# Optimization experiments

Hardware: AMD Instinct MI355X
Metric: run time of the kernel (lower is better)

Reference implementation:

```python
import jax, jax.numpy as jnp
import numpy as np

B, K, H, W = 8, 1024, 24, 24
C = H * W            # in_channels = 576
NH = 6               # hardcoded num_heads
HD = C // NH         # 96


def setup_inputs() -> dict:
    key = jax.random.key(0)
    ks = jax.random.split(key, 8)
    s = 1.0 / np.sqrt(C)
    return {
        "input1": jax.random.normal(ks[0], (B, K, H, W), jnp.float32),
        "input2": jax.random.normal(ks[1], (B, K, H, W), jnp.float32),
        "Wq": jax.random.uniform(ks[2], (C, C), jnp.float32, -s, s),
        "bq": jax.random.uniform(ks[3], (C,), jnp.float32, -s, s),
        "Wk": jax.random.uniform(ks[4], (C, C), jnp.float32, -s, s),
        "bk": jax.random.uniform(ks[5], (C,), jnp.float32, -s, s),
        "Wv": jax.random.uniform(ks[6], (C, C), jnp.float32, -s, s),
        "bv": jax.random.uniform(ks[7], (C,), jnp.float32, -s, s),
    }


def reference(input1, input2, Wq, bq, Wk, bk, Wv, bv):
    b, k, h, w = input1.shape
    c = h * w
    x1 = input1.reshape(b, k, c)
    x2 = input2.reshape(b, k, c)
    # torch nn.Linear: y = x @ W^T + b
    q = x1 @ Wq.T + bq                      # [b, k, c]
    kk = x2 @ Wk.T + bk
    v = x2 @ Wv.T + bv
    # torch .view scrambles: [b, k, c] -> [b, NH, c//NH, k] (row-major reshape)
    q = q.reshape(b, NH, c // NH, k)
    kk = kk.reshape(b, NH, c // NH, k)
    v = v.reshape(b, NH, c // NH, k)
    # scores = q^T k over head-dim; NOTE: no 1/sqrt(d) scaling in original
    scores = jnp.einsum('bhdq,bhdk->bhqk', q, kk)   # [b, NH, k, k]
    weights = jax.nn.softmax(scores, axis=-1)
    # context = value @ weights^T -> [b, NH, hd, k]
    ctx = jnp.einsum('bhdk,bhqk->bhdq', v, weights)
    return ctx.reshape(b, k, h, w)
```

## Files before the change

### kernel.cpp

```cpp
#include <hip/hip_runtime.h>
#include <cmath>

#define BATCH 8
#define KDIM  1024
#define CH    576
#define NHEAD 6
#define HDIM  96

typedef _Float16 f16;
typedef f16 f16x4 __attribute__((ext_vector_type(4)));
typedef f16 f16x8 __attribute__((ext_vector_type(8)));
typedef float f32x16 __attribute__((ext_vector_type(16)));
typedef unsigned int u32;

__device__ inline f32x16 zero16() {
    f32x16 z;
#pragma unroll
    for (int r = 0; r < 16; ++r) z[r] = 0.f;
    return z;
}

__global__ __launch_bounds__(256) void proj_kernel(
    const float* __restrict__ x1, const float* __restrict__ x2,
    const float* __restrict__ Wq, const float* __restrict__ Wk,
    const float* __restrict__ Wv,
    const float* __restrict__ bq, const float* __restrict__ bk,
    const float* __restrict__ bv,
    f16* __restrict__ qf, f16* __restrict__ kf, f16* __restrict__ vf)
{
    const int z = blockIdx.z;
    const float* A    = (z == 0) ? x1 : x2;
    const float* W    = (z == 0) ? Wq : (z == 1) ? Wk : Wv;
    const float* bias = (z == 0) ? bq : (z == 1) ? bk : bv;
    f16* dst          = (z == 0) ? qf : (z == 1) ? kf : vf;

    __shared__ f16 As[128 * 72];
    __shared__ f16 Ws[96 * 72];

    const int tid = threadIdx.x;
    const int lane = tid & 63, w = tid >> 6;
    const int l31 = lane & 31, half = lane >> 5;
    const int nBase = blockIdx.x * 96;
    const int mBase = blockIdx.y * 128;

    f32x16 acc[3] = {zero16(), zero16(), zero16()};

    for (int k0 = 0; k0 < CH; k0 += 64) {
        __syncthreads();
#pragma unroll
        for (int r = 0; r < 4; ++r) {
            int idx = r * 256 + tid;
            int row = idx >> 3, ch = idx & 7;
            const float* src = &A[(size_t)(mBase + row) * CH + k0 + ch * 8];
            float4 u0 = *(const float4*)src;
            float4 u1 = *(const float4*)(src + 4);
            f16x8 hv;
            hv[0] = (f16)u0.x; hv[1] = (f16)u0.y; hv[2] = (f16)u0.z; hv[3] = (f16)u0.w;
            hv[4] = (f16)u1.x; hv[5] = (f16)u1.y; hv[6] = (f16)u1.z; hv[7] = (f16)u1.w;
            *(f16x8*)&As[row * 72 + ch * 8] = hv;
        }
#pragma unroll
        for (int r = 0; r < 3; ++r) {
            int idx = r * 256 + tid;
            int row = idx >> 3, ch = idx & 7;
            const float* src = &W[(size_t)(nBase + row) * CH + k0 + ch * 8];
            float4 u0 = *(const float4*)src;
            float4 u1 = *(const float4*)(src + 4);
            f16x8 hv;
            hv[0] = (f16)u0.x; hv[1] = (f16)u0.y; hv[2] = (f16)u0.z; hv[3] = (f16)u0.w;
            hv[4] = (f16)u1.x; hv[5] = (f16)u1.y; hv[6] = (f16)u1.z; hv[7] = (f16)u1.w;
            *(f16x8*)&Ws[row * 72 + ch * 8] = hv;
        }
        __syncthreads();
#pragma unroll
        for (int ks = 0; ks < 4; ++ks) {
            f16x8 a = *(const f16x8*)&As[(32 * w + l31) * 72 + 16 * ks + 8 * half];
#pragma unroll
            for (int nt = 0; nt < 3; ++nt) {
                f16x8 bfr = *(const f16x8*)&Ws[(32 * nt + l31) * 72 + 16 * ks + 8 * half];
                acc[nt] = __builtin_amdgcn_mfma_f32_32x32x16_f16(a, bfr, acc[nt], 0, 0, 0);
            }
        }
    }

#pragma unroll
    for (int nt = 0; nt < 3; ++nt) {
        int n = nBase + 32 * nt + l31;
        float bsv = bias[n];
#pragma unroll
        for (int r = 0; r < 16; ++r) {
            int m = mBase + 32 * w + (r & 3) + 8 * (r >> 2) + 4 * half;
            dst[(size_t)m * CH + n] = (f16)(acc[nt][r] + bsv);
        }
    }
}

__global__ __launch_bounds__(256) void transpose_qk(
    const f16* __restrict__ qf, const f16* __restrict__ kf,
    f16* __restrict__ QT, f16* __restrict__ KT)
{
    const int tt = blockIdx.x;
    const int bh = blockIdx.y;
    const f16* src = blockIdx.z ? kf : qf;
    f16* dst = blockIdx.z ? KT : QT;

    __shared__ f16 Ts[96 * 72];

    const int tid = threadIdx.x;
    const int rowbase = (bh / NHEAD) * CH + (bh % NHEAD) * HDIM;

#pragma unroll
    for (int r = 0; r < 3; ++r) {
        int idx = r * 256 + tid;
        int d = idx >> 3, g = idx & 7;
        *(f16x8*)&Ts[d * 72 + g * 8] =
            *(const f16x8*)&src[(size_t)(rowbase + d) * KDIM + tt * 64 + g * 8];
    }
    __syncthreads();
#pragma unroll
    for (int r = 0; r < 3; ++r) {
        int idx = r * 256 + tid;
        int t = idx & 63, dg = idx >> 6;
        f16x8 v;
#pragma unroll
        for (int u = 0; u < 8; ++u) v[u] = Ts[(dg * 8 + u) * 72 + t];
        *(f16x8*)&dst[((size_t)bh * KDIM + tt * 64 + t) * HDIM + dg * 8] = v;
    }
}

__global__ __launch_bounds__(256, 3) void attn_kernel(
    const f16* __restrict__ qT, const f16* __restrict__ kT,
    const f16* __restrict__ vf, float* __restrict__ out)
{
    __shared__ __align__(16) char smem[27136];
    f16* Ks = (f16*)smem;
    f16* Vs = (f16*)(smem + 13312);
    f16* Qs = Ks;

    const int qt = blockIdx.x;
    const int h  = blockIdx.y;
    const int b  = blockIdx.z;
    const int bh = b * NHEAD + h;

    const int tid = threadIdx.x;
    const int lane = tid & 63, w = tid >> 6;
    const int ih = w & 1, jg = w >> 1;
    const int l31 = lane & 31, half = lane >> 5;
    const int iw = 32 * ih;

    const f16* Qbase = qT + ((size_t)bh * KDIM + qt * 64) * HDIM;
    const f16* Kbase = kT + (size_t)bh * KDIM * HDIM;
    const f16* Vbase = vf + ((size_t)b * CH + (size_t)h * HDIM) * KDIM;

    int kt[3], kg[3], vd[3], vg[3];
#pragma unroll
    for (int r = 0; r < 3; ++r) {
        int idx = r * 256 + tid;
        kt[r] = idx / 12; kg[r] = idx % 12;
        vd[r] = idx >> 3; vg[r] = idx & 7;
    }

#pragma unroll
    for (int r = 0; r < 3; ++r)
        *(f16x8*)&Qs[kt[r] * 104 + kg[r] * 8] =
            *(const f16x8*)&Qbase[kt[r] * 96 + kg[r] * 8];
    __syncthreads();
    f16x8 qfr[6];
#pragma unroll
    for (int ks = 0; ks < 6; ++ks)
        qfr[ks] = *(const f16x8*)&Qs[(iw + l31) * 104 + 16 * ks + 8 * half];

    f16x8 kreg[3], vreg[3];
#pragma unroll
    for (int r = 0; r < 3; ++r) {
        kreg[r] = *(const f16x8*)&Kbase[(size_t)kt[r] * HDIM + kg[r] * 8];
        vreg[r] = *(const f16x8*)&Vbase[(size_t)vd[r] * KDIM + vg[r] * 8];
    }

    float m_run = -INFINITY, l_run = 0.f;
    f32x16 Oacc[3] = {zero16(), zero16(), zero16()};

    for (int jt = 0; jt < KDIM; jt += 64) {
        __syncthreads();
#pragma unroll
        for (int r = 0; r < 3; ++r) {
            *(f16x8*)&Ks[kt[r] * 104 + kg[r] * 8] = kreg[r];
            *(f16x8*)&Vs[vd[r] * 72 + vg[r] * 8]  = vreg[r];
        }
        __syncthreads();
        if (jt + 64 < KDIM) {
#pragma unroll
            for (int r = 0; r < 3; ++r) {
                kreg[r] = *(const f16x8*)&Kbase[(size_t)(jt + 64 + kt[r]) * HDIM + kg[r] * 8];
                vreg[r] = *(const f16x8*)&Vbase[(size_t)vd[r] * KDIM + jt + 64 + vg[r] * 8];
            }
        }

        f32x16 s0 = zero16();
#pragma unroll
        for (int ks = 0; ks < 6; ++ks) {
            f16x8 ak = *(const f16x8*)&Ks[(32 * jg + l31) * 104 + 16 * ks + 8 * half];
            s0 = __builtin_amdgcn_mfma_f32_32x32x16_f16(ak, qfr[ks], s0, 0, 0, 0);
        }

        float mx = -INFINITY;
#pragma unroll
        for (int r = 0; r < 16; ++r) mx = fmaxf(mx, s0[r]);
        mx = fmaxf(mx, __shfl_xor(mx, 32));
        float mnew = fmaxf(m_run, mx);
        float alpha = __expf(m_run - mnew);
        m_run = mnew;
        float sum = 0.f;
        f16x4 pq[4];
#pragma unroll
        for (int r = 0; r < 16; ++r) {
            float e = __expf(s0[r] - mnew);
            sum += e;
            pq[r >> 2][r & 3] = (f16)e;
        }
        sum += __shfl_xor(sum, 32);
        l_run = alpha * l_run + sum;

        if (__any(alpha != 1.0f)) {
#pragma unroll
            for (int t = 0; t < 3; ++t)
#pragma unroll
                for (int r = 0; r < 16; ++r) Oacc[t][r] *= alpha;
        }

#pragma unroll
        for (int kc = 0; kc < 2; ++kc) {
            union { f16x4 h; u32 u[2]; } snd, rcv, keep;
            keep.h = half ? pq[2 * kc + 1] : pq[2 * kc];
            snd.h  = half ? pq[2 * kc]     : pq[2 * kc + 1];
            rcv.u[0] = __shfl_xor((int)snd.u[0], 32);
            rcv.u[1] = __shfl_xor((int)snd.u[1], 32);
            f16x8 bp;
            if (half == 0) {
#pragma unroll
                for (int v = 0; v < 4; ++v) { bp[v] = keep.h[v]; bp[4 + v] = rcv.h[v]; }
            } else {
#pragma unroll
                for (int v = 0; v < 4; ++v) { bp[v] = rcv.h[v]; bp[4 + v] = keep.h[v]; }
            }
            int jo = 32 * jg + 16 * kc + 8 * half;
#pragma unroll
            for (int t = 0; t < 3; ++t) {
                f16x8 av = *(const f16x8*)&Vs[(32 * t + l31) * 72 + jo];
                Oacc[t] = __builtin_amdgcn_mfma_f32_32x32x16_f16(av, bp, Oacc[t], 0, 0, 0);
            }
        }
    }

    __syncthreads();
    float* Oscr = (float*)smem;
    float* mScr = (float*)(smem + 25344);
    float* lScr = (float*)(smem + 25600);
    if (jg == 1) {
        if (half == 0) { mScr[iw + l31] = m_run; lScr[iw + l31] = l_run; }
        float* od = Oscr + ih * 3168;
#pragma unroll
        for (int t = 0; t < 3; ++t)
#pragma unroll
            for (int r = 0; r < 16; ++r) {
                int d = 32 * t + (r & 3) + 8 * (r >> 2) + 4 * half;
                od[d * 33 + l31] = Oacc[t][r];
            }
    }
    __syncthreads();
    if (jg == 0) {
        float m1 = mScr[iw + l31], l1 = lScr[iw + l31];
        float mstar = fmaxf(m_run, m1);
        float a0 = __expf(m_run - mstar), a1 = __expf(m1 - mstar);
        float linv = 1.0f / (l_run * a0 + l1 * a1);
        const float* od = Oscr + ih * 3168;
        float* obase = out + ((size_t)b * CH + (size_t)h * HDIM) * KDIM
                           + qt * 64 + iw + l31;
#pragma unroll
        for (int t = 0; t < 3; ++t)
#pragma unroll
            for (int r = 0; r < 16; ++r) {
                int d = 32 * t + (r & 3) + 8 * (r >> 2) + 4 * half;
                obase[(size_t)d * KDIM] =
                    (Oacc[t][r] * a0 + od[d * 33 + l31] * a1) * linv;
            }
    }
}

extern "C" void kernel_launch(void* const* d_in, const int* in_sizes, int n_in,
                              void* d_out, int out_size, void* d_ws, size_t ws_size,
                              hipStream_t stream)
{
    const float* x1 = (const float*)d_in[0];
    const float* x2 = (const float*)d_in[1];
    const float* Wq = (const float*)d_in[2];
    const float* bq = (const float*)d_in[3];
    const float* Wk = (const float*)d_in[4];
    const float* bk = (const float*)d_in[5];
    const float* Wv = (const float*)d_in[6];
    const float* bv = (const float*)d_in[7];
    float* out = (float*)d_out;

    const size_t P = (size_t)BATCH * KDIM * CH;
    f16* qf = (f16*)d_ws;
    f16* kf = qf + P;
    f16* vf = kf + P;
    f16* QT = vf + P;
    f16* KT = QT + P;

    dim3 pgrid(CH / 96, (BATCH * KDIM) / 128, 3);
    proj_kernel<<<pgrid, 256, 0, stream>>>(x1, x2, Wq, Wk, Wv,
                                           bq, bk, bv, qf, kf, vf);

    dim3 tgrid(KDIM / 64, BATCH * NHEAD, 2);
    transpose_qk<<<tgrid, 256, 0, stream>>>(qf, kf, QT, KT);

    dim3 agrid(KDIM / 64, NHEAD, BATCH);
    attn_kernel<<<agrid, 256, 0, stream>>>(QT, KT, vf, out);
}
```

Before: 190.4 us.

## Pre-convert inputs and weights to fp16, widen projection N-tile to 192

Adds a separate conversion kernel that casts x1, x2 and the three weight matrices to fp16 once. The projection GEMM then loads fp16 directly and covers 192 output columns per block instead of 96, so each A tile is reused across six MFMA column tiles. This removes the fp32 load-and-convert work from the GEMM inner loop and halves how often the activations are re-read per N-tile. In exchange it adds an extra kernel launch and a full fp32 read plus fp16 write of the inputs, and uses more LDS and accumulator registers per block. The workspace is reorganised so the fp16 input buffers are reused for the transposed Q/K.

```diff
diff --git a/kernel.cpp b/kernel.cpp
--- a/kernel.cpp
+++ b/kernel.cpp
@@ -13,6 +13,9 @@
 typedef float f32x16 __attribute__((ext_vector_type(16)));
 typedef unsigned int u32;
 
+#define PSZ  (BATCH * KDIM * CH)
+#define WSZ  (CH * CH)
+
 __device__ inline f32x16 zero16() {
     f32x16 z;
 #pragma unroll
@@ -20,30 +23,61 @@
     return z;
 }
 
-__global__ __launch_bounds__(256) void proj_kernel(
+__global__ __launch_bounds__(256) void convert_kernel(
     const float* __restrict__ x1, const float* __restrict__ x2,
     const float* __restrict__ Wq, const float* __restrict__ Wk,
     const float* __restrict__ Wv,
+    f16* __restrict__ x1h, f16* __restrict__ x2h, f16* __restrict__ wh)
+{
+    const int y = blockIdx.y;
+    int idx = blockIdx.x * 256 + threadIdx.x;
+    const float* src;
+    f16* dst;
+    if (y == 0) {
+        if (idx >= PSZ / 8) return;
+        src = x1; dst = x1h;
+    } else if (y == 1) {
+        if (idx >= PSZ / 8) return;
+        src = x2; dst = x2h;
+    } else {
+        if (idx >= 3 * WSZ / 8) return;
+        int seg = idx / (WSZ / 8);
+        src = (seg == 0) ? Wq : (seg == 1) ? Wk : Wv;
+        dst = wh + seg * WSZ;
+        idx -= seg * (WSZ / 8);
+        if (y > 2) return;
+    }
+    float4 u0 = ((const float4*)src)[2 * idx];
+    float4 u1 = ((const float4*)src)[2 * idx + 1];
+    f16x8 hv;
+    hv[0] = (f16)u0.x; hv[1] = (f16)u0.y; hv[2] = (f16)u0.z; hv[3] = (f16)u0.w;
+    hv[4] = (f16)u1.x; hv[5] = (f16)u1.y; hv[6] = (f16)u1.z; hv[7] = (f16)u1.w;
+    ((f16x8*)dst)[idx] = hv;
+}
+
+__global__ __launch_bounds__(256) void proj_kernel(
+    const f16* __restrict__ x1h, const f16* __restrict__ x2h,
+    const f16* __restrict__ wh,
     const float* __restrict__ bq, const float* __restrict__ bk,
     const float* __restrict__ bv,
     f16* __restrict__ qf, f16* __restrict__ kf, f16* __restrict__ vf)
 {
     const int z = blockIdx.z;
-    const float* A    = (z == 0) ? x1 : x2;
-    const float* W    = (z == 0) ? Wq : (z == 1) ? Wk : Wv;
+    const f16* A     = (z == 0) ? x1h : x2h;
+    const f16* W     = wh + z * WSZ;
     const float* bias = (z == 0) ? bq : (z == 1) ? bk : bv;
     f16* dst          = (z == 0) ? qf : (z == 1) ? kf : vf;
 
     __shared__ f16 As[128 * 72];
-    __shared__ f16 Ws[96 * 72];
+    __shared__ f16 Ws[192 * 72];
 
     const int tid = threadIdx.x;
     const int lane = tid & 63, w = tid >> 6;
     const int l31 = lane & 31, half = lane >> 5;
-    const int nBase = blockIdx.x * 96;
+    const int nBase = blockIdx.x * 192;
     const int mBase = blockIdx.y * 128;
 
-    f32x16 acc[3] = {zero16(), zero16(), zero16()};
+    f32x16 acc[6] = {zero16(), zero16(), zero16(), zero16(), zero16(), zero16()};
 
     for (int k0 = 0; k0 < CH; k0 += 64) {
         __syncthreads();
@@ -51,32 +85,22 @@
         for (int r = 0; r < 4; ++r) {
             int idx = r * 256 + tid;
             int row = idx >> 3, ch = idx & 7;
-            const float* src = &A[(size_t)(mBase + row) * CH + k0 + ch * 8];
-            float4 u0 = *(const float4*)src;
-            float4 u1 = *(const float4*)(src + 4);
-            f16x8 hv;
-            hv[0] = (f16)u0.x; hv[1] = (f16)u0.y; hv[2] = (f16)u0.z; hv[3] = (f16)u0.w;
-            hv[4] = (f16)u1.x; hv[5] = (f16)u1.y; hv[6] = (f16)u1.z; hv[7] = (f16)u1.w;
-            *(f16x8*)&As[row * 72 + ch * 8] = hv;
-        }
-#pragma unroll
-        for (int r = 0; r < 3; ++r) {
+            *(f16x8*)&As[row * 72 + ch * 8] =
+                *(const f16x8*)&A[(size_t)(mBase + row) * CH + k0 + ch * 8];
+        }
+#pragma unroll
+        for (int r = 0; r < 6; ++r) {
             int idx = r * 256 + tid;
             int row = idx >> 3, ch = idx & 7;
-            const float* src = &W[(size_t)(nBase + row) * CH + k0 + ch * 8];
-            float4 u0 = *(const float4*)src;
-            float4 u1 = *(const float4*)(src + 4);
-            f16x8 hv;
-            hv[0] = (f16)u0.x; hv[1] = (f16)u0.y; hv[2] = (f16)u0.z; hv[3] = (f16)u0.w;
-            hv[4] = (f16)u1.x; hv[5] = (f16)u1.y; hv[6] = (f16)u1.z; hv[7] = (f16)u1.w;
-            *(f16x8*)&Ws[row * 72 + ch * 8] = hv;
+            *(f16x8*)&Ws[row * 72 + ch * 8] =
+                *(const f16x8*)&W[(size_t)(nBase + row) * CH + k0 + ch * 8];
         }
         __syncthreads();
 #pragma unroll
         for (int ks = 0; ks < 4; ++ks) {
             f16x8 a = *(const f16x8*)&As[(32 * w + l31) * 72 + 16 * ks + 8 * half];
 #pragma unroll
-            for (int nt = 0; nt < 3; ++nt) {
+            for (int nt = 0; nt < 6; ++nt) {
                 f16x8 bfr = *(const f16x8*)&Ws[(32 * nt + l31) * 72 + 16 * ks + 8 * half];
                 acc[nt] = __builtin_amdgcn_mfma_f32_32x32x16_f16(a, bfr, acc[nt], 0, 0, 0);
             }
@@ -84,7 +108,7 @@
     }
 
 #pragma unroll
-    for (int nt = 0; nt < 3; ++nt) {
+    for (int nt = 0; nt < 6; ++nt) {
         int n = nBase + 32 * nt + l31;
         float bsv = bias[n];
 #pragma unroll
@@ -301,16 +325,21 @@
     const float* bv = (const float*)d_in[7];
     float* out = (float*)d_out;
 
-    const size_t P = (size_t)BATCH * KDIM * CH;
-    f16* qf = (f16*)d_ws;
-    f16* kf = qf + P;
-    f16* vf = kf + P;
-    f16* QT = vf + P;
-    f16* KT = QT + P;
-
-    dim3 pgrid(CH / 96, (BATCH * KDIM) / 128, 3);
-    proj_kernel<<<pgrid, 256, 0, stream>>>(x1, x2, Wq, Wk, Wv,
-                                           bq, bk, bv, qf, kf, vf);
+    const size_t P = PSZ;
+    f16* x1h = (f16*)d_ws;
+    f16* x2h = x1h + P;
+    f16* qf  = x2h + P;
+    f16* kf  = qf + P;
+    f16* vf  = kf + P;
+    f16* wh  = vf + P;
+    f16* QT  = x1h;
+    f16* KT  = x2h;
+
+    dim3 cgrid((P / 8 + 255) / 256, 3);
+    convert_kernel<<<cgrid, 256, 0, stream>>>(x1, x2, Wq, Wk, Wv, x1h, x2h, wh);
+
+    dim3 pgrid(CH / 192, (BATCH * KDIM) / 128, 3);
+    proj_kernel<<<pgrid, 256, 0, stream>>>(x1h, x2h, wh, bq, bk, bv, qf, kf, vf);
 
     dim3 tgrid(KDIM / 64, BATCH * NHEAD, 2);
     transpose_qk<<<tgrid, 256, 0, stream>>>(qf, kf, QT, KT);
```

After: 175.9 us. 1.08x faster.
